# Performance work log

Measured on AMD Instinct MI355X. Metric: run time of the kernel, lower is better.

The kernel has to match this reference:

```python
import jax, jax.numpy as jnp
import numpy as np

B, S, H = 8, 4096, 1024
N_GATHER = 65536
NUM_SEGMENTS = 16384


def setup_inputs() -> dict:
    key = jax.random.key(0)
    ks = jax.random.split(key, 7)
    transformer_hidden = jax.random.normal(ks[0], (B, S, H), dtype=jnp.float32)
    dense_w = jax.random.normal(ks[1], (H, H), dtype=jnp.float32) * (1.0 / np.sqrt(H))
    dense_b = jax.random.normal(ks[2], (H,), dtype=jnp.float32) * 0.02
    proj_w = jax.random.normal(ks[3], (H,), dtype=jnp.float32) * (1.0 / np.sqrt(H))
    proj_b = jax.random.normal(ks[4], (1,), dtype=jnp.float32) * 0.02
    flat_indices = jax.random.randint(ks[5], (N_GATHER,), 0, B * S, dtype=jnp.int32)
    segment_ids = jnp.sort(jax.random.randint(ks[6], (N_GATHER,), 0, NUM_SEGMENTS, dtype=jnp.int32))
    return {
        "transformer_hidden": transformer_hidden,
        "dense_w": dense_w,
        "dense_b": dense_b,
        "proj_w": proj_w,
        "proj_b": proj_b,
        "flat_indices": flat_indices,
        "segment_ids": segment_ids,
    }


def reference(transformer_hidden, dense_w, dense_b, proj_w, proj_b, flat_indices, segment_ids):
    # Flatten [B,S,H] -> [B*S,H] and gather per-object token hidden states.
    flat = transformer_hidden.reshape(-1, H)
    gathered = flat[flat_indices]  # [N_GATHER, H]
    # Ragged per-group mean (variable-length index sets).
    sums = jax.ops.segment_sum(gathered, segment_ids, num_segments=NUM_SEGMENTS)  # [G, H]
    counts = jax.ops.segment_sum(
        jnp.ones((N_GATHER,), dtype=gathered.dtype), segment_ids, num_segments=NUM_SEGMENTS
    )
    h = sums / jnp.maximum(counts, 1.0)[:, None]  # [G, H]
    # dense -> gelu -> linear head (torch F.gelu is exact, not tanh approx)
    z = jax.nn.gelu(h @ dense_w.T + dense_b, approximate=False)
    predictions = z @ proj_w + proj_b  # [G]
    return predictions.reshape(-1)
```

## Files before the change

kernel.cpp:

```cpp
#include <hip/hip_runtime.h>

#define H 1024
#define NG 65536
#define NSEG 16384

#define BM 256
#define BN 256
#define BK 64
#define NT (H / BK)

typedef __attribute__((ext_vector_type(8))) short bf16x8;
typedef __attribute__((ext_vector_type(4))) float f32x4;

__device__ __forceinline__ unsigned short f2bf(float x) {
    unsigned u = __builtin_bit_cast(unsigned, x);
    unsigned r = (u + 0x7fffu + ((u >> 16) & 1u)) >> 16;
    return (unsigned short)r;
}

__device__ __forceinline__ void gload_lds16(const void* g, void* l) {
    __builtin_amdgcn_global_load_lds(
        (const __attribute__((address_space(1))) void*)g,
        (__attribute__((address_space(3))) void*)l, 16, 0, 0);
}

#define CFENCE() asm volatile("" ::: "memory")

__global__ void setup_kernel(const float* __restrict__ w, unsigned short* __restrict__ wbf,
                             const float* __restrict__ proj_b, float* __restrict__ out,
                             const int* __restrict__ seg, int* __restrict__ seg_start) {
    int b = blockIdx.x;
    if (b < 1024) {
        int i = (b * 256 + threadIdx.x) * 4;
        float4 v = *(const float4*)(w + i);
        ushort4 o;
        o.x = f2bf(v.x); o.y = f2bf(v.y); o.z = f2bf(v.z); o.w = f2bf(v.w);
        *(ushort4*)(wbf + i) = o;
    } else if (b < 1088) {
        int i = (b - 1024) * 256 + threadIdx.x;
        if (i < NSEG) out[i] = proj_b[0];
    } else {
        int g = (b - 1088) * 256 + threadIdx.x;
        if (g > NSEG) return;
        if (g == NSEG) { seg_start[g] = NG; return; }
        int lo = 0, hi = NG;
        while (lo < hi) { int mid = (lo + hi) >> 1; if (seg[mid] < g) lo = mid + 1; else hi = mid; }
        seg_start[g] = lo;
    }
}

__global__ void seg_mean_kernel(const float* __restrict__ hidden,
                                const int* __restrict__ flat_indices,
                                const int* __restrict__ seg_start,
                                unsigned short* __restrict__ hbf) {
    int g = blockIdx.x;
    int t = threadIdx.x;
    int s = seg_start[g], e = seg_start[g + 1];
    float4 acc = {0.f, 0.f, 0.f, 0.f};
    for (int i = s; i < e; ++i) {
        int row = flat_indices[i];
        float4 v = *((const float4*)(hidden + (size_t)row * H) + t);
        acc.x += v.x; acc.y += v.y; acc.z += v.z; acc.w += v.w;
    }
    float scale = (e > s) ? 1.0f / (float)(e - s) : 0.0f;
    ushort4 o;
    o.x = f2bf(acc.x * scale); o.y = f2bf(acc.y * scale);
    o.z = f2bf(acc.z * scale); o.w = f2bf(acc.w * scale);
    *(ushort4*)(hbf + (size_t)g * H + t * 4) = o;
}

__global__ __launch_bounds__(512, 2) void gemm_kernel(
    const unsigned short* __restrict__ Abf,
    const unsigned short* __restrict__ Wbf,
    const float* __restrict__ dense_b,
    const float* __restrict__ proj_w,
    float* __restrict__ out) {
    __shared__ unsigned short As[2][BM * BK];
    __shared__ unsigned short Bs[2][BN * BK];
    const int tid = threadIdx.x;
    const int wid = tid >> 6, lane = tid & 63;
    const int wr = wid >> 2, wc = wid & 3;
    const int m0 = blockIdx.x * BM, n0 = blockIdx.y * BN;

    f32x4 acc[8][4] = {};

    auto STAGE = [&](int buf, int kt) {
#pragma unroll
        for (int it = 0; it < 4; ++it) {
            int c = it * 512 + tid;
            int row = c >> 3;
            int sw = ((c & 7) << 4) ^ ((row & 7) << 4);
            gload_lds16((const char*)Abf + (((size_t)(m0 + row)) << 11) + kt * 128 + sw,
                        (char*)&As[buf][0] + (it * 512 + wid * 64) * 16);
        }
#pragma unroll
        for (int it = 0; it < 4; ++it) {
            int c = it * 512 + tid;
            int row = c >> 3;
            int sw = ((c & 7) << 4) ^ ((row & 7) << 4);
            gload_lds16((const char*)Wbf + (((size_t)(n0 + row)) << 11) + kt * 128 + sw,
                        (char*)&Bs[buf][0] + (it * 512 + wid * 64) * 16);
        }
    };

    STAGE(0, 0);

    for (int t = 0; t < NT; ++t) {
        CFENCE();
        __builtin_amdgcn_s_barrier();
        CFENCE();
        if (t + 1 < NT) {
            STAGE((t + 1) & 1, t + 1);
            asm volatile("s_waitcnt vmcnt(8)" ::: "memory");
        } else {
            asm volatile("s_waitcnt vmcnt(0)" ::: "memory");
        }
        __builtin_amdgcn_s_barrier();
        CFENCE();

        const char* Ab = (const char*)&As[t & 1][0];
        const char* Bb = (const char*)&Bs[t & 1][0];
        __builtin_amdgcn_s_setprio(1);
#pragma unroll
        for (int kk = 0; kk < 2; ++kk) {
            bf16x8 af[8], bw[4];
            int kb = kk * 64 + ((lane >> 4) << 4);
#pragma unroll
            for (int ni = 0; ni < 4; ++ni) {
                int row = wc * 64 + ni * 16 + (lane & 15);
                bw[ni] = *(const bf16x8*)(Bb + row * 128 + (kb ^ ((row & 7) << 4)));
            }
#pragma unroll
            for (int mi = 0; mi < 8; ++mi) {
                int row = wr * 128 + mi * 16 + (lane & 15);
                af[mi] = *(const bf16x8*)(Ab + row * 128 + (kb ^ ((row & 7) << 4)));
            }
#pragma unroll
            for (int mi = 0; mi < 8; ++mi)
#pragma unroll
                for (int ni = 0; ni < 4; ++ni)
                    acc[mi][ni] = __builtin_amdgcn_mfma_f32_16x16x32_bf16(af[mi], bw[ni], acc[mi][ni], 0, 0, 0);
        }
        __builtin_amdgcn_s_setprio(0);
    }

    float db[4], pw[4];
#pragma unroll
    for (int ni = 0; ni < 4; ++ni) {
        int n = n0 + wc * 64 + ni * 16 + (lane & 15);
        db[ni] = dense_b[n];
        pw[ni] = proj_w[n];
    }
#pragma unroll
    for (int mi = 0; mi < 8; ++mi) {
#pragma unroll
        for (int r = 0; r < 4; ++r) {
            int m = m0 + wr * 128 + mi * 16 + ((lane >> 4) << 2) + r;
            float s = 0.f;
#pragma unroll
            for (int ni = 0; ni < 4; ++ni) {
                float z = acc[mi][ni][r] + db[ni];
                float gl = 0.5f * z * (1.0f + erff(z * 0.70710678118f));
                s += gl * pw[ni];
            }
#pragma unroll
            for (int off = 1; off < 16; off <<= 1) s += __shfl_xor(s, off, 64);
            if ((lane & 15) == 0) atomicAdd(out + m, s);
        }
    }
}

extern "C" void kernel_launch(void* const* d_in, const int* in_sizes, int n_in,
                              void* d_out, int out_size, void* d_ws, size_t ws_size,
                              hipStream_t stream) {
    const float* hidden       = (const float*)d_in[0];
    const float* dense_w      = (const float*)d_in[1];
    const float* dense_b      = (const float*)d_in[2];
    const float* proj_w       = (const float*)d_in[3];
    const float* proj_b       = (const float*)d_in[4];
    const int*   flat_indices = (const int*)d_in[5];
    const int*   segment_ids  = (const int*)d_in[6];
    float* out = (float*)d_out;

    char* ws = (char*)d_ws;
    int* seg_start = (int*)ws;
    unsigned short* hbf = (unsigned short*)(ws + (1 << 17));
    unsigned short* wbf = (unsigned short*)(ws + (1 << 17) + (size_t)NSEG * H * 2);

    hipLaunchKernelGGL(setup_kernel, dim3(1153), dim3(256), 0, stream,
                       dense_w, wbf, proj_b, out, segment_ids, seg_start);
    hipLaunchKernelGGL(seg_mean_kernel, dim3(NSEG), dim3(256), 0, stream,
                       hidden, flat_indices, seg_start, hbf);
    hipLaunchKernelGGL(gemm_kernel, dim3(NSEG / BM, H / BN), dim3(512), 0, stream,
                       hbf, wbf, dense_b, proj_w, out);
}
```

Measured before the change: 103.5 us.

## Fuse segment-mean gather into GEMM with per-block full-N loop, drop atomics

```diff
diff --git a/kernel.cpp b/kernel.cpp
--- a/kernel.cpp
+++ b/kernel.cpp
@@ -4,10 +4,10 @@
 #define NG 65536
 #define NSEG 16384
 
-#define BM 256
-#define BN 256
-#define BK 64
-#define NT (H / BK)
+#define FBM 64
+#define FBN 256
+#define FBK 64
+#define NSTEP 64
 
 typedef __attribute__((ext_vector_type(8))) short bf16x8;
 typedef __attribute__((ext_vector_type(4))) float f32x4;
@@ -27,7 +27,6 @@
 #define CFENCE() asm volatile("" ::: "memory")
 
 __global__ void setup_kernel(const float* __restrict__ w, unsigned short* __restrict__ wbf,
-                             const float* __restrict__ proj_b, float* __restrict__ out,
                              const int* __restrict__ seg, int* __restrict__ seg_start) {
     int b = blockIdx.x;
     if (b < 1024) {
@@ -36,11 +35,8 @@
         ushort4 o;
         o.x = f2bf(v.x); o.y = f2bf(v.y); o.z = f2bf(v.z); o.w = f2bf(v.w);
         *(ushort4*)(wbf + i) = o;
-    } else if (b < 1088) {
-        int i = (b - 1024) * 256 + threadIdx.x;
-        if (i < NSEG) out[i] = proj_b[0];
     } else {
-        int g = (b - 1088) * 256 + threadIdx.x;
+        int g = (b - 1024) * 256 + threadIdx.x;
         if (g > NSEG) return;
         if (g == NSEG) { seg_start[g] = NG; return; }
         int lo = 0, hi = NG;
@@ -49,81 +45,99 @@
     }
 }
 
-__global__ void seg_mean_kernel(const float* __restrict__ hidden,
-                                const int* __restrict__ flat_indices,
-                                const int* __restrict__ seg_start,
-                                unsigned short* __restrict__ hbf) {
-    int g = blockIdx.x;
-    int t = threadIdx.x;
-    int s = seg_start[g], e = seg_start[g + 1];
-    float4 acc = {0.f, 0.f, 0.f, 0.f};
-    for (int i = s; i < e; ++i) {
-        int row = flat_indices[i];
-        float4 v = *((const float4*)(hidden + (size_t)row * H) + t);
-        acc.x += v.x; acc.y += v.y; acc.z += v.z; acc.w += v.w;
-    }
-    float scale = (e > s) ? 1.0f / (float)(e - s) : 0.0f;
-    ushort4 o;
-    o.x = f2bf(acc.x * scale); o.y = f2bf(acc.y * scale);
-    o.z = f2bf(acc.z * scale); o.w = f2bf(acc.w * scale);
-    *(ushort4*)(hbf + (size_t)g * H + t * 4) = o;
-}
-
-__global__ __launch_bounds__(512, 2) void gemm_kernel(
-    const unsigned short* __restrict__ Abf,
+__global__ __launch_bounds__(512, 2) void fused_kernel(
+    const float* __restrict__ hidden,
+    const int* __restrict__ flat_indices,
+    const int* __restrict__ seg_start,
     const unsigned short* __restrict__ Wbf,
     const float* __restrict__ dense_b,
     const float* __restrict__ proj_w,
+    const float* __restrict__ proj_b,
+    unsigned short* __restrict__ hbf,
     float* __restrict__ out) {
-    __shared__ unsigned short As[2][BM * BK];
-    __shared__ unsigned short Bs[2][BN * BK];
+    __shared__ unsigned short As[2][FBM * FBK];
+    __shared__ unsigned short Bs[2][FBN * FBK];
     const int tid = threadIdx.x;
+    const int bid = blockIdx.x;
+    const int r0 = bid * FBM;
+
+    {
+        int team = tid >> 8;
+        int tt = tid & 255;
+        for (int s = 0; s < 32; ++s) {
+            int g = r0 + team * 32 + s;
+            int st = seg_start[g], en = seg_start[g + 1];
+            float4 a = {0.f, 0.f, 0.f, 0.f};
+            for (int i = st; i < en; ++i) {
+                int row = flat_indices[i];
+                float4 v = *((const float4*)(hidden + (size_t)row * H) + tt);
+                a.x += v.x; a.y += v.y; a.z += v.z; a.w += v.w;
+            }
+            float sc = (en > st) ? 1.0f / (float)(en - st) : 0.0f;
+            ushort4 o;
+            o.x = f2bf(a.x * sc); o.y = f2bf(a.y * sc);
+            o.z = f2bf(a.z * sc); o.w = f2bf(a.w * sc);
+            *(ushort4*)(hbf + (size_t)g * H + tt * 4) = o;
+        }
+    }
+    __syncthreads();
+
     const int wid = tid >> 6, lane = tid & 63;
     const int wr = wid >> 2, wc = wid & 3;
-    const int m0 = blockIdx.x * BM, n0 = blockIdx.y * BN;
-
-    f32x4 acc[8][4] = {};
-
-    auto STAGE = [&](int buf, int kt) {
+
+    auto STAGE = [&](int buf, int step) {
+        int nc = step >> 4, kt = step & 15;
+        {
+            int c = tid;
+            int row = c >> 3;
+            int sw = ((c & 7) << 4) ^ ((row & 7) << 4);
+            gload_lds16((const char*)hbf + (((size_t)(r0 + row)) << 11) + kt * 128 + sw,
+                        (char*)&As[buf][0] + (wid * 64) * 16);
+        }
 #pragma unroll
         for (int it = 0; it < 4; ++it) {
             int c = it * 512 + tid;
             int row = c >> 3;
             int sw = ((c & 7) << 4) ^ ((row & 7) << 4);
-            gload_lds16((const char*)Abf + (((size_t)(m0 + row)) << 11) + kt * 128 + sw,
-                        (char*)&As[buf][0] + (it * 512 + wid * 64) * 16);
-        }
-#pragma unroll
-        for (int it = 0; it < 4; ++it) {
-            int c = it * 512 + tid;
-            int row = c >> 3;
-            int sw = ((c & 7) << 4) ^ ((row & 7) << 4);
-            gload_lds16((const char*)Wbf + (((size_t)(n0 + row)) << 11) + kt * 128 + sw,
+            gload_lds16((const char*)Wbf + (((size_t)(nc * FBN + row)) << 11) + kt * 128 + sw,
                         (char*)&Bs[buf][0] + (it * 512 + wid * 64) * 16);
         }
     };
 
+    f32x4 acc[2][4] = {};
+    float p[2][4] = {};
+    float db[4], pw[4];
+
     STAGE(0, 0);
-
-    for (int t = 0; t < NT; ++t) {
+    for (int s = 0; s < NSTEP; ++s) {
+        int kt = s & 15;
+        if (kt == 0) {
+            int nc = s >> 4;
+#pragma unroll
+            for (int ni = 0; ni < 4; ++ni) {
+                int n = nc * FBN + wc * 64 + ni * 16 + (lane & 15);
+                db[ni] = dense_b[n];
+                pw[ni] = proj_w[n];
+            }
+        }
         CFENCE();
         __builtin_amdgcn_s_barrier();
         CFENCE();
-        if (t + 1 < NT) {
-            STAGE((t + 1) & 1, t + 1);
-            asm volatile("s_waitcnt vmcnt(8)" ::: "memory");
+        if (s + 1 < NSTEP) {
+            STAGE((s + 1) & 1, s + 1);
+            asm volatile("s_waitcnt vmcnt(5)" ::: "memory");
         } else {
             asm volatile("s_waitcnt vmcnt(0)" ::: "memory");
         }
         __builtin_amdgcn_s_barrier();
         CFENCE();
 
-        const char* Ab = (const char*)&As[t & 1][0];
-        const char* Bb = (const char*)&Bs[t & 1][0];
+        const char* Ab = (const char*)&As[s & 1][0];
+        const char* Bb = (const char*)&Bs[s & 1][0];
         __builtin_amdgcn_s_setprio(1);
 #pragma unroll
         for (int kk = 0; kk < 2; ++kk) {
-            bf16x8 af[8], bw[4];
+            bf16x8 af[2], bw[4];
             int kb = kk * 64 + ((lane >> 4) << 4);
 #pragma unroll
             for (int ni = 0; ni < 4; ++ni) {
@@ -131,42 +145,61 @@
                 bw[ni] = *(const bf16x8*)(Bb + row * 128 + (kb ^ ((row & 7) << 4)));
             }
 #pragma unroll
-            for (int mi = 0; mi < 8; ++mi) {
-                int row = wr * 128 + mi * 16 + (lane & 15);
+            for (int mi = 0; mi < 2; ++mi) {
+                int row = wr * 32 + mi * 16 + (lane & 15);
                 af[mi] = *(const bf16x8*)(Ab + row * 128 + (kb ^ ((row & 7) << 4)));
             }
 #pragma unroll
-            for (int mi = 0; mi < 8; ++mi)
+            for (int mi = 0; mi < 2; ++mi)
 #pragma unroll
                 for (int ni = 0; ni < 4; ++ni)
                     acc[mi][ni] = __builtin_amdgcn_mfma_f32_16x16x32_bf16(af[mi], bw[ni], acc[mi][ni], 0, 0, 0);
         }
         __builtin_amdgcn_s_setprio(0);
-    }
-
-    float db[4], pw[4];
-#pragma unroll
-    for (int ni = 0; ni < 4; ++ni) {
-        int n = n0 + wc * 64 + ni * 16 + (lane & 15);
-        db[ni] = dense_b[n];
-        pw[ni] = proj_w[n];
-    }
-#pragma unroll
-    for (int mi = 0; mi < 8; ++mi) {
+
+        if (kt == 15) {
+#pragma unroll
+            for (int mi = 0; mi < 2; ++mi)
+#pragma unroll
+                for (int r = 0; r < 4; ++r) {
+                    float sacc = 0.f;
+#pragma unroll
+                    for (int ni = 0; ni < 4; ++ni) {
+                        float z = acc[mi][ni][r] + db[ni];
+                        float gl = 0.5f * z * (1.0f + erff(z * 0.70710678118f));
+                        sacc += gl * pw[ni];
+                    }
+                    p[mi][r] += sacc;
+#pragma unroll
+                    for (int ni = 0; ni < 4; ++ni) acc[mi][ni][r] = 0.f;
+                }
+        }
+    }
+
+#pragma unroll
+    for (int mi = 0; mi < 2; ++mi)
 #pragma unroll
         for (int r = 0; r < 4; ++r) {
-            int m = m0 + wr * 128 + mi * 16 + ((lane >> 4) << 2) + r;
-            float s = 0.f;
-#pragma unroll
-            for (int ni = 0; ni < 4; ++ni) {
-                float z = acc[mi][ni][r] + db[ni];
-                float gl = 0.5f * z * (1.0f + erff(z * 0.70710678118f));
-                s += gl * pw[ni];
-            }
-#pragma unroll
-            for (int off = 1; off < 16; off <<= 1) s += __shfl_xor(s, off, 64);
-            if ((lane & 15) == 0) atomicAdd(out + m, s);
-        }
+            float v = p[mi][r];
+#pragma unroll
+            for (int off = 1; off < 16; off <<= 1) v += __shfl_xor(v, off, 64);
+            p[mi][r] = v;
+        }
+    __syncthreads();
+    float* scratch = (float*)&As[0][0];
+    if ((lane & 15) == 0) {
+#pragma unroll
+        for (int mi = 0; mi < 2; ++mi)
+#pragma unroll
+            for (int r = 0; r < 4; ++r) {
+                int lr = wr * 32 + mi * 16 + ((lane >> 4) << 2) + r;
+                scratch[wc * 64 + lr] = p[mi][r];
+            }
+    }
+    __syncthreads();
+    if (tid < FBM) {
+        float v = proj_b[0] + scratch[tid] + scratch[64 + tid] + scratch[128 + tid] + scratch[192 + tid];
+        out[r0 + tid] = v;
     }
 }
 
@@ -187,10 +220,8 @@
     unsigned short* hbf = (unsigned short*)(ws + (1 << 17));
     unsigned short* wbf = (unsigned short*)(ws + (1 << 17) + (size_t)NSEG * H * 2);
 
-    hipLaunchKernelGGL(setup_kernel, dim3(1153), dim3(256), 0, stream,
-                       dense_w, wbf, proj_b, out, segment_ids, seg_start);
-    hipLaunchKernelGGL(seg_mean_kernel, dim3(NSEG), dim3(256), 0, stream,
-                       hidden, flat_indices, seg_start, hbf);
-    hipLaunchKernelGGL(gemm_kernel, dim3(NSEG / BM, H / BN), dim3(512), 0, stream,
-                       hbf, wbf, dense_b, proj_w, out);
-}
+    hipLaunchKernelGGL(setup_kernel, dim3(1089), dim3(256), 0, stream,
+                       dense_w, wbf, segment_ids, seg_start);
+    hipLaunchKernelGGL(fused_kernel, dim3(256), dim3(512), 0, stream,
+                       hidden, flat_indices, seg_start, wbf, dense_b, proj_w, proj_b, hbf, out);
+}
```

Result: slower. 176.1 us (+70.2%).

## Assign one wavefront per segment with shuffled indices and 4-row unrolled gathers

Applied to the files above, without the earlier changes.

```diff
diff --git a/kernel.cpp b/kernel.cpp
--- a/kernel.cpp
+++ b/kernel.cpp
@@ -53,20 +53,56 @@
                                 const int* __restrict__ flat_indices,
                                 const int* __restrict__ seg_start,
                                 unsigned short* __restrict__ hbf) {
-    int g = blockIdx.x;
-    int t = threadIdx.x;
+    int g = (blockIdx.x << 2) + (threadIdx.x >> 6);
+    int lane = threadIdx.x & 63;
     int s = seg_start[g], e = seg_start[g + 1];
-    float4 acc = {0.f, 0.f, 0.f, 0.f};
-    for (int i = s; i < e; ++i) {
-        int row = flat_indices[i];
-        float4 v = *((const float4*)(hidden + (size_t)row * H) + t);
-        acc.x += v.x; acc.y += v.y; acc.z += v.z; acc.w += v.w;
-    }
-    float scale = (e > s) ? 1.0f / (float)(e - s) : 0.0f;
-    ushort4 o;
-    o.x = f2bf(acc.x * scale); o.y = f2bf(acc.y * scale);
-    o.z = f2bf(acc.z * scale); o.w = f2bf(acc.w * scale);
-    *(ushort4*)(hbf + (size_t)g * H + t * 4) = o;
+    int len = e - s;
+
+    float4 acc[4] = {{0.f,0.f,0.f,0.f},{0.f,0.f,0.f,0.f},{0.f,0.f,0.f,0.f},{0.f,0.f,0.f,0.f}};
+
+    for (int base = 0; base < len; base += 64) {
+        int nb = len - base; if (nb > 64) nb = 64;
+        int idx = (base + lane < len) ? flat_indices[s + base + lane] : 0;
+        int i = 0;
+        for (; i + 4 <= nb; i += 4) {
+            int r0 = __shfl(idx, i, 64);
+            int r1 = __shfl(idx, i + 1, 64);
+            int r2 = __shfl(idx, i + 2, 64);
+            int r3 = __shfl(idx, i + 3, 64);
+            const float4* p0 = (const float4*)(hidden + (size_t)r0 * H) + lane;
+            const float4* p1 = (const float4*)(hidden + (size_t)r1 * H) + lane;
+            const float4* p2 = (const float4*)(hidden + (size_t)r2 * H) + lane;
+            const float4* p3 = (const float4*)(hidden + (size_t)r3 * H) + lane;
+            float4 v0[4], v1[4], v2[4], v3[4];
+#pragma unroll
+            for (int c = 0; c < 4; ++c) { v0[c] = p0[c * 64]; v1[c] = p1[c * 64]; v2[c] = p2[c * 64]; v3[c] = p3[c * 64]; }
+#pragma unroll
+            for (int c = 0; c < 4; ++c) {
+                acc[c].x += v0[c].x + v1[c].x + v2[c].x + v3[c].x;
+                acc[c].y += v0[c].y + v1[c].y + v2[c].y + v3[c].y;
+                acc[c].z += v0[c].z + v1[c].z + v2[c].z + v3[c].z;
+                acc[c].w += v0[c].w + v1[c].w + v2[c].w + v3[c].w;
+            }
+        }
+        for (; i < nb; ++i) {
+            int r = __shfl(idx, i, 64);
+            const float4* p = (const float4*)(hidden + (size_t)r * H) + lane;
+#pragma unroll
+            for (int c = 0; c < 4; ++c) {
+                float4 v = p[c * 64];
+                acc[c].x += v.x; acc[c].y += v.y; acc[c].z += v.z; acc[c].w += v.w;
+            }
+        }
+    }
+
+    float sc = (len > 0) ? 1.0f / (float)len : 0.0f;
+#pragma unroll
+    for (int c = 0; c < 4; ++c) {
+        ushort4 o;
+        o.x = f2bf(acc[c].x * sc); o.y = f2bf(acc[c].y * sc);
+        o.z = f2bf(acc[c].z * sc); o.w = f2bf(acc[c].w * sc);
+        *(ushort4*)(hbf + (size_t)g * H + c * 256 + lane * 4) = o;
+    }
 }
 
 __global__ __launch_bounds__(512, 2) void gemm_kernel(
@@ -189,7 +225,7 @@
 
     hipLaunchKernelGGL(setup_kernel, dim3(1153), dim3(256), 0, stream,
                        dense_w, wbf, proj_b, out, segment_ids, seg_start);
-    hipLaunchKernelGGL(seg_mean_kernel, dim3(NSEG), dim3(256), 0, stream,
+    hipLaunchKernelGGL(seg_mean_kernel, dim3(NSEG / 4), dim3(256), 0, stream,
                        hidden, flat_indices, seg_start, hbf);
     hipLaunchKernelGGL(gemm_kernel, dim3(NSEG / BM, H / BN), dim3(512), 0, stream,
                        hbf, wbf, dense_b, proj_w, out);
```

New measurement: 106.1 us. 1.03x slower.
